# Performance work log

Hardware: AMD Instinct MI355X
Metric: run time of the kernel (lower is better)

Reference implementation:

```python
import jax, jax.numpy as jnp
import numpy as np

MAX_BITS = 64
HIDDEN = 256
EPS = 1e-5
TEMPERATURE = 1.0  # buffer default


def _layernorm(x, gamma, beta):
    mu = jnp.mean(x, axis=-1, keepdims=True)
    var = jnp.var(x, axis=-1, keepdims=True)
    return (x - mu) * jax.lax.rsqrt(var + EPS) * gamma + beta


def setup_inputs() -> dict:
    key = jax.random.key(0)
    ks = jax.random.split(key, 8)
    B = 32768
    # binary-ish inputs in [0,1)
    a_bits = (jax.random.uniform(ks[0], (B, MAX_BITS)) < 0.5).astype(jnp.float32)
    shift_bits = (jax.random.uniform(ks[1], (B, MAX_BITS)) < 0.5).astype(jnp.float32)
    # decoder: Linear(64,256) -> LN -> ReLU -> Linear(256,256) -> LN -> ReLU -> Linear(256,64)
    def lin(k, out_d, in_d):
        bound = 1.0 / np.sqrt(in_d)
        kw, kb = jax.random.split(k)
        W = jax.random.uniform(kw, (out_d, in_d), minval=-bound, maxval=bound)
        b = jax.random.uniform(kb, (out_d,), minval=-bound, maxval=bound)
        return W, b
    W1, b1 = lin(ks[2], HIDDEN, MAX_BITS)
    W2, b2 = lin(ks[3], HIDDEN, HIDDEN)
    W3, b3 = lin(ks[4], MAX_BITS, HIDDEN)
    g1 = jnp.ones((HIDDEN,)); be1 = jnp.zeros((HIDDEN,))
    g2 = jnp.ones((HIDDEN,)); be2 = jnp.zeros((HIDDEN,))
    return {
        "a_bits": a_bits, "shift_bits": shift_bits,
        "W1": W1, "b1": b1, "g1": g1, "be1": be1,
        "W2": W2, "b2": b2, "g2": g2, "be2": be2,
        "W3": W3, "b3": b3,
    }


def reference(a_bits, shift_bits, W1, b1, g1, be1, W2, b2, g2, be2, W3, b3):
    bits = a_bits.shape[1]
    # 2-layer MLP decoder
    h = jax.nn.relu(_layernorm(shift_bits @ W1.T + b1, g1, be1))
    h = jax.nn.relu(_layernorm(h @ W2.T + b2, g2, be2))
    shift_logits = (h @ W3.T + b3)[:, :bits]
    # training path: softmax over shift positions
    shift_probs = jax.nn.softmax(shift_logits / TEMPERATURE, axis=-1)
    # Toeplitz shift-sum: out[b,i] = sum_{s<=i} probs[b,s] * a_bits[b,i-s]
    i = jnp.arange(bits)[:, None]
    s = jnp.arange(bits)[None, :]
    idx = i - s                       # [bits, bits]
    mask = (idx >= 0)
    gath = a_bits[:, jnp.where(mask, idx, 0)] * mask.astype(a_bits.dtype)  # [B, bits, bits]
    return jnp.einsum('bis,bs->bi', gath, shift_probs)
```

## Files before the change

### kernel.cpp

```cpp
#include <hip/hip_runtime.h>
#include <hip/hip_fp16.h>


typedef short s8v __attribute__((ext_vector_type(8)));
typedef float f4v __attribute__((ext_vector_type(4)));

#define HPAD 264
#define PPAD 68

#define OFF_W1F 0
#define OFF_W2F 16384
#define OFF_W3F 81920
#define OFF_B1  98304
#define OFF_G1  98560
#define OFF_BE1 98816
#define OFF_B2  99072
#define OFF_G2  99328
#define OFF_BE2 99584
#define OFF_B3  99840

__device__ __forceinline__ float b2f(unsigned short u) {
    union { unsigned int i; float f; } v; v.i = ((unsigned int)u) << 16; return v.f;
}
__device__ __forceinline__ unsigned short f2b(float f) {
    union { float f; unsigned int i; } v; v.f = f;
    return (unsigned short)((v.i + 0x7fffu + ((v.i >> 16) & 1u)) >> 16);
}
__device__ __forceinline__ unsigned int cvtpk(float a, float b) {
    unsigned int r;
    asm("v_cvt_pk_bf16_f32 %0, %1, %2" : "=v"(r) : "v"(a), "v"(b));
    return r;
}
__device__ __forceinline__ int h2i(__half2 h) { union { __half2 h; int i; } u; u.h = h; return u.i; }
__device__ __forceinline__ __half2 i2h(int i) { union { __half2 h; int i; } u; u.i = i; return u.h; }

__device__ __forceinline__ bool probe_bf16(const void* a_bits) {
    unsigned int wv = ((const unsigned int*)a_bits)[threadIdx.x & 63];
    return __ballot((wv & 0xffffu) == 0x3f80u) != 0ULL;
}

__global__ __launch_bounds__(256) void convert_kernel(
    const void* __restrict__ a_probe,
    const void* __restrict__ W1, const void* __restrict__ W2, const void* __restrict__ W3,
    const void* __restrict__ b1, const void* __restrict__ g1, const void* __restrict__ be1,
    const void* __restrict__ b2, const void* __restrict__ g2, const void* __restrict__ be2,
    const void* __restrict__ b3,
    unsigned short* __restrict__ ws)
{
    const bool isbf = probe_bf16(a_probe);
    const int t = blockIdx.x * 256 + threadIdx.x;

    if (t < 12288) {
        const void* W; int K, idx, dstbase;
        if (t < 2048)       { idx = t;         W = W1; K = 64;  dstbase = OFF_W1F + idx * 8; }
        else if (t < 10240) { idx = t - 2048;  W = W2; K = 256; dstbase = OFF_W2F + idx * 8; }
        else                { idx = t - 10240; W = W3; K = 256; dstbase = OFF_W3F + idx * 8; }
        int nt, kc, lane;
        if (t < 2048) { nt = idx >> 7; kc = (idx >> 6) & 1; lane = idx & 63; }
        else          { nt = idx >> 9; kc = (idx >> 6) & 7; lane = idx & 63; }
        const int row = nt * 16 + (lane & 15);
        const int col = kc * 32 + (lane >> 4) * 8;
        const int src = row * K + col;
        s8v o;
        if (isbf) {
            o = *(const s8v*)((const unsigned short*)W + src);
        } else {
            const float* f = (const float*)W + src;
#pragma unroll
            for (int j = 0; j < 8; ++j) o[j] = (short)f2b(f[j]);
        }
        *(s8v*)(ws + dstbase) = o;
    } else if (t < 12488) {
        const int v = t - 12288;
        const void* srcp; int base, off;
        if (v < 32)       { srcp = b1;  base = OFF_B1;  off = v * 8; }
        else if (v < 64)  { srcp = g1;  base = OFF_G1;  off = (v - 32) * 8; }
        else if (v < 96)  { srcp = be1; base = OFF_BE1; off = (v - 64) * 8; }
        else if (v < 128) { srcp = b2;  base = OFF_B2;  off = (v - 96) * 8; }
        else if (v < 160) { srcp = g2;  base = OFF_G2;  off = (v - 128) * 8; }
        else if (v < 192) { srcp = be2; base = OFF_BE2; off = (v - 160) * 8; }
        else              { srcp = b3;  base = OFF_B3;  off = (v - 192) * 8; }
#pragma unroll
        for (int j = 0; j < 8; ++j)
            ws[base + off + j] = isbf ? ((const unsigned short*)srcp)[off + j]
                                      : f2b(((const float*)srcp)[off + j]);
    }
}

template<bool BF16>
__device__ __forceinline__ float loadS(const void* p, int idx) {
    if constexpr (BF16) return b2f(((const unsigned short*)p)[idx]);
    else return ((const float*)p)[idx];
}
template<bool BF16>
__device__ __forceinline__ s8v loadA8(const void* p, int idx) {
    if constexpr (BF16) {
        return *(const s8v*)((const unsigned short*)p + idx);
    } else {
        const float* f = (const float*)p + idx;
        f4v a = *(const f4v*)f;
        f4v b = *(const f4v*)(f + 4);
        union { s8v s; unsigned int u[4]; } r;
        r.u[0] = cvtpk(a[0], a[1]);
        r.u[1] = cvtpk(a[2], a[3]);
        r.u[2] = cvtpk(b[0], b[1]);
        r.u[3] = cvtpk(b[2], b[3]);
        return r.s;
    }
}
template<bool BF16>
__device__ __forceinline__ void storeO(void* p, int idx, float v) {
    if constexpr (BF16) ((unsigned short*)p)[idx] = f2b(v);
    else ((float*)p)[idx] = v;
}

__device__ __forceinline__ void ln_relu_store(
    f4v* acc, const unsigned short* ws, int offB, int offG, int offBe,
    short* Hs, float* SS, int w, int q, int c, int row, int ntb)
{
    float sm[4][4], sv[4][4];
#pragma unroll
    for (int mt = 0; mt < 4; ++mt)
#pragma unroll
        for (int r = 0; r < 4; ++r) { sm[mt][r] = 0.f; sv[mt][r] = 0.f; }
#pragma unroll
    for (int i = 0; i < 4; ++i) {
        const float bias = b2f(ws[offB + (ntb + i) * 16 + c]);
#pragma unroll
        for (int mt = 0; mt < 4; ++mt)
#pragma unroll
            for (int r = 0; r < 4; ++r) {
                float v = acc[mt * 4 + i][r] + bias;
                acc[mt * 4 + i][r] = v;
                sm[mt][r] += v; sv[mt][r] += v * v;
            }
    }
#pragma unroll
    for (int m = 1; m <= 8; m <<= 1)
#pragma unroll
        for (int mt = 0; mt < 4; ++mt)
#pragma unroll
            for (int r = 0; r < 4; ++r) {
                sm[mt][r] += __shfl_xor(sm[mt][r], m, 64);
                sv[mt][r] += __shfl_xor(sv[mt][r], m, 64);
            }
    if (c == 0)
#pragma unroll
        for (int mt = 0; mt < 4; ++mt)
#pragma unroll
            for (int r = 0; r < 4; ++r) {
                const int g = mt * 16 + row + r;
                *(float2*)&SS[g * 8 + w * 2] = make_float2(sm[mt][r], sv[mt][r]);
            }
    __syncthreads();
#pragma unroll
    for (int mt = 0; mt < 4; ++mt)
#pragma unroll
        for (int r = 0; r < 4; ++r) {
            const int g = mt * 16 + row + r;
            f4v v0 = *(const f4v*)&SS[g * 8];
            f4v v1 = *(const f4v*)&SS[g * 8 + 4];
            float st = v0[0] + v0[2] + v1[0] + v1[2];
            float sq = v0[1] + v0[3] + v1[1] + v1[3];
            float mean = st * (1.0f / 256.0f);
            float var  = fmaxf(sq * (1.0f / 256.0f) - mean * mean, 0.0f);
            sm[mt][r] = mean; sv[mt][r] = rsqrtf(var + 1e-5f);
        }
#pragma unroll
    for (int i = 0; i < 4; ++i) {
        const int nt = ntb + i;
        const float gg = b2f(ws[offG + nt * 16 + c]);
        const float bb = b2f(ws[offBe + nt * 16 + c]);
#pragma unroll
        for (int mt = 0; mt < 4; ++mt) {
            float y[4];
#pragma unroll
            for (int r = 0; r < 4; ++r)
                y[r] = fmaxf((acc[mt * 4 + i][r] - sm[mt][r]) * sv[mt][r] * gg + bb, 0.0f);
            unsigned int u01 = cvtpk(y[0], y[1]);
            unsigned int u23 = cvtpk(y[2], y[3]);
            Hs[(mt * 16 + row + 0) * HPAD + nt * 16 + c] = (short)(u01 & 0xffffu);
            Hs[(mt * 16 + row + 1) * HPAD + nt * 16 + c] = (short)(u01 >> 16);
            Hs[(mt * 16 + row + 2) * HPAD + nt * 16 + c] = (short)(u23 & 0xffffu);
            Hs[(mt * 16 + row + 3) * HPAD + nt * 16 + c] = (short)(u23 >> 16);
        }
    }
}

template<bool BF16>
__device__ __forceinline__ void pipeline(
    const void* a_bits, const void* shifts, const unsigned short* ws, void* out,
    short* Hs, float* Ps, float* SS)
{
    const int tid = threadIdx.x;
    const int w = tid >> 6;
    const int l = tid & 63;
    const int q = l >> 4;
    const int c = l & 15;
    const int ntb = w << 2;
    const int grow0 = (int)blockIdx.x << 6;
    const int row = q * 4;

    f4v acc1[16];
#pragma unroll
    for (int i = 0; i < 16; ++i) acc1[i] = (f4v){0.f, 0.f, 0.f, 0.f};

    s8v xa[4][2];
#pragma unroll
    for (int mt = 0; mt < 4; ++mt) {
        xa[mt][0] = loadA8<BF16>(shifts, (grow0 + mt * 16 + c) * 64 + q * 8);
        xa[mt][1] = loadA8<BF16>(shifts, (grow0 + mt * 16 + c) * 64 + 32 + q * 8);
    }
#pragma unroll
    for (int i = 0; i < 4; ++i) {
        const int nt = ntb + i;
        s8v wb0 = *(const s8v*)(ws + OFF_W1F + ((nt * 2 + 0) * 64 + l) * 8);
        s8v wb1 = *(const s8v*)(ws + OFF_W1F + ((nt * 2 + 1) * 64 + l) * 8);
#pragma unroll
        for (int mt = 0; mt < 4; ++mt) {
            acc1[mt * 4 + i] = __builtin_amdgcn_mfma_f32_16x16x32_bf16(xa[mt][0], wb0, acc1[mt * 4 + i], 0, 0, 0);
            acc1[mt * 4 + i] = __builtin_amdgcn_mfma_f32_16x16x32_bf16(xa[mt][1], wb1, acc1[mt * 4 + i], 0, 0, 0);
        }
    }
    ln_relu_store(acc1, ws, OFF_B1, OFF_G1, OFF_BE1, Hs, SS, w, q, c, row, ntb);
    __syncthreads();

    f4v acc2[16];
#pragma unroll
    for (int i = 0; i < 16; ++i) acc2[i] = (f4v){0.f, 0.f, 0.f, 0.f};
#pragma unroll
    for (int ks = 0; ks < 8; ++ks) {
        s8v af[4];
#pragma unroll
        for (int mt = 0; mt < 4; ++mt)
            af[mt] = *(const s8v*)&Hs[(mt * 16 + c) * HPAD + ks * 32 + q * 8];
#pragma unroll
        for (int i = 0; i < 4; ++i) {
            s8v bf_ = *(const s8v*)(ws + OFF_W2F + (((ntb + i) * 8 + ks) * 64 + l) * 8);
#pragma unroll
            for (int mt = 0; mt < 4; ++mt)
                acc2[mt * 4 + i] = __builtin_amdgcn_mfma_f32_16x16x32_bf16(af[mt], bf_, acc2[mt * 4 + i], 0, 0, 0);
        }
    }
    ln_relu_store(acc2, ws, OFF_B2, OFF_G2, OFF_BE2, Hs, SS, w, q, c, row, ntb);
    __syncthreads();

    f4v acc3[4];
#pragma unroll
    for (int t = 0; t < 4; ++t) acc3[t] = (f4v){0.f, 0.f, 0.f, 0.f};
#pragma unroll
    for (int ks = 0; ks < 8; ++ks) {
        s8v bf_ = *(const s8v*)(ws + OFF_W3F + ((w * 8 + ks) * 64 + l) * 8);
#pragma unroll
        for (int mt = 0; mt < 4; ++mt) {
            s8v af = *(const s8v*)&Hs[(mt * 16 + c) * HPAD + ks * 32 + q * 8];
            acc3[mt] = __builtin_amdgcn_mfma_f32_16x16x32_bf16(af, bf_, acc3[mt], 0, 0, 0);
        }
    }
    {
        const float bias = b2f(ws[OFF_B3 + w * 16 + c]);
        float sum[4][4];
#pragma unroll
        for (int mt = 0; mt < 4; ++mt)
#pragma unroll
            for (int r = 0; r < 4; ++r) {
                float e = __expf(acc3[mt][r] + bias);
                Ps[(mt * 16 + row + r) * PPAD + w * 16 + c] = e;
                sum[mt][r] = e;
            }
#pragma unroll
        for (int m = 1; m <= 8; m <<= 1)
#pragma unroll
            for (int mt = 0; mt < 4; ++mt)
#pragma unroll
                for (int r = 0; r < 4; ++r)
                    sum[mt][r] += __shfl_xor(sum[mt][r], m, 64);
        if (c == 0)
#pragma unroll
            for (int mt = 0; mt < 4; ++mt)
#pragma unroll
                for (int r = 0; r < 4; ++r)
                    SS[(mt * 16 + row + r) * 8 + w * 2 + 1] = sum[mt][r];
    }
    __syncthreads();

#pragma unroll
    for (int jj = 0; jj < 8; ++jj) {
        const int m0 = w * 16 + jj;
        const int m1 = m0 + 8;
        f4v u0 = *(const f4v*)&SS[m0 * 8];
        f4v u1 = *(const f4v*)&SS[m0 * 8 + 4];
        f4v u2 = *(const f4v*)&SS[m1 * 8];
        f4v u3 = *(const f4v*)&SS[m1 * 8 + 4];
        const float i0 = __builtin_amdgcn_rcpf(u0[1] + u0[3] + u1[1] + u1[3]);
        const float i1 = __builtin_amdgcn_rcpf(u2[1] + u2[3] + u3[1] + u3[3]);
        __half2 pph = __floats2half2_rn(Ps[m0 * PPAD + l] * i0,
                                        Ps[m1 * PPAD + l] * i1);
        const int ppi = h2i(pph);
        __half2 aah = __floats2half2_rn(loadS<BF16>(a_bits, (grow0 + m0) * 64 + l),
                                        loadS<BF16>(a_bits, (grow0 + m1) * 64 + l));
        int rr = h2i(aah);
        __half2 acc = __float2half2_rn(0.0f);
#pragma unroll
        for (int s = 0; s < 64; ++s) {
            const int spi = __builtin_amdgcn_readlane(ppi, s);
            acc = __hfma2(i2h(spi), i2h(rr), acc);
            if (s < 63)
                rr = __builtin_amdgcn_update_dpp(0, rr, 0x138, 0xF, 0xF, true);
        }
        storeO<BF16>(out, (grow0 + m0) * 64 + l, __low2float(acc));
        storeO<BF16>(out, (grow0 + m1) * 64 + l, __high2float(acc));
    }
}

__global__ __launch_bounds__(256, 3) void shiftdec_kernel(
    const void* __restrict__ a_bits, const void* __restrict__ shifts,
    const unsigned short* __restrict__ ws, void* __restrict__ out)
{
    __shared__ __align__(16) short Hs[64 * HPAD];
    __shared__ __align__(16) float Ps[64 * PPAD];
    __shared__ __align__(16) float SSb[64 * 8];

    if (probe_bf16(a_bits))
        pipeline<true>(a_bits, shifts, ws, out, Hs, Ps, SSb);
    else
        pipeline<false>(a_bits, shifts, ws, out, Hs, Ps, SSb);
}

extern "C" void kernel_launch(void* const* d_in, const int* in_sizes, int n_in,
                              void* d_out, int out_size, void* d_ws, size_t ws_size,
                              hipStream_t stream) {
    const int B = in_sizes[0] / 64;
    const int grid = B / 64;

    hipLaunchKernelGGL(convert_kernel, dim3(49), dim3(256), 0, stream,
                       d_in[0], d_in[2], d_in[6], d_in[10],
                       d_in[3], d_in[4], d_in[5], d_in[7], d_in[8], d_in[9], d_in[11],
                       (unsigned short*)d_ws);
    hipLaunchKernelGGL(shiftdec_kernel, dim3(grid), dim3(256), 0, stream,
                       d_in[0], d_in[1], (const unsigned short*)d_ws, d_out);
}
```

Baseline: 123.2 us.

## Split each 64-row tile across eight waves instead of four

Doubles the block to 512 threads so each wave owns two output column tiles instead of four in the two hidden layers. The last layer is split by column tile and row pair, and the shift-sum loop covers fewer rows per wave. LayerNorm partial stats now combine eight waves, and the softmax sums use a new shared buffer. This halves accumulator registers per thread to raise occupancy and parallelism per tile. The cost is more cross-wave reduction and barrier traffic, and each wave reuses the loaded A fragments over fewer MFMAs.

After: 132.0 us. 1.07x slower.

```diff
diff --git a/kernel.cpp b/kernel.cpp
--- a/kernel.cpp
+++ b/kernel.cpp
@@ -124,14 +124,14 @@
 #pragma unroll
         for (int r = 0; r < 4; ++r) { sm[mt][r] = 0.f; sv[mt][r] = 0.f; }
 #pragma unroll
-    for (int i = 0; i < 4; ++i) {
+    for (int i = 0; i < 2; ++i) {
         const float bias = b2f(ws[offB + (ntb + i) * 16 + c]);
 #pragma unroll
         for (int mt = 0; mt < 4; ++mt)
 #pragma unroll
             for (int r = 0; r < 4; ++r) {
-                float v = acc[mt * 4 + i][r] + bias;
-                acc[mt * 4 + i][r] = v;
+                float v = acc[mt * 2 + i][r] + bias;
+                acc[mt * 2 + i][r] = v;
                 sm[mt][r] += v; sv[mt][r] += v * v;
             }
     }
@@ -150,7 +150,7 @@
 #pragma unroll
             for (int r = 0; r < 4; ++r) {
                 const int g = mt * 16 + row + r;
-                *(float2*)&SS[g * 8 + w * 2] = make_float2(sm[mt][r], sv[mt][r]);
+                *(float2*)&SS[g * 16 + w * 2] = make_float2(sm[mt][r], sv[mt][r]);
             }
     __syncthreads();
 #pragma unroll
@@ -158,16 +158,18 @@
 #pragma unroll
         for (int r = 0; r < 4; ++r) {
             const int g = mt * 16 + row + r;
-            f4v v0 = *(const f4v*)&SS[g * 8];
-            f4v v1 = *(const f4v*)&SS[g * 8 + 4];
-            float st = v0[0] + v0[2] + v1[0] + v1[2];
-            float sq = v0[1] + v0[3] + v1[1] + v1[3];
+            f4v v0 = *(const f4v*)&SS[g * 16];
+            f4v v1 = *(const f4v*)&SS[g * 16 + 4];
+            f4v v2 = *(const f4v*)&SS[g * 16 + 8];
+            f4v v3 = *(const f4v*)&SS[g * 16 + 12];
+            float st = (v0[0] + v0[2]) + (v1[0] + v1[2]) + (v2[0] + v2[2]) + (v3[0] + v3[2]);
+            float sq = (v0[1] + v0[3]) + (v1[1] + v1[3]) + (v2[1] + v2[3]) + (v3[1] + v3[3]);
             float mean = st * (1.0f / 256.0f);
             float var  = fmaxf(sq * (1.0f / 256.0f) - mean * mean, 0.0f);
             sm[mt][r] = mean; sv[mt][r] = rsqrtf(var + 1e-5f);
         }
 #pragma unroll
-    for (int i = 0; i < 4; ++i) {
+    for (int i = 0; i < 2; ++i) {
         const int nt = ntb + i;
         const float gg = b2f(ws[offG + nt * 16 + c]);
         const float bb = b2f(ws[offBe + nt * 16 + c]);
@@ -176,7 +178,7 @@
             float y[4];
 #pragma unroll
             for (int r = 0; r < 4; ++r)
-                y[r] = fmaxf((acc[mt * 4 + i][r] - sm[mt][r]) * sv[mt][r] * gg + bb, 0.0f);
+                y[r] = fmaxf((acc[mt * 2 + i][r] - sm[mt][r]) * sv[mt][r] * gg + bb, 0.0f);
             unsigned int u01 = cvtpk(y[0], y[1]);
             unsigned int u23 = cvtpk(y[2], y[3]);
             Hs[(mt * 16 + row + 0) * HPAD + nt * 16 + c] = (short)(u01 & 0xffffu);
@@ -190,20 +192,20 @@
 template<bool BF16>
 __device__ __forceinline__ void pipeline(
     const void* a_bits, const void* shifts, const unsigned short* ws, void* out,
-    short* Hs, float* Ps, float* SS)
+    short* Hs, float* Ps, float* SS, float* SM)
 {
     const int tid = threadIdx.x;
     const int w = tid >> 6;
     const int l = tid & 63;
     const int q = l >> 4;
     const int c = l & 15;
-    const int ntb = w << 2;
+    const int ntb = w << 1;
     const int grow0 = (int)blockIdx.x << 6;
     const int row = q * 4;
 
-    f4v acc1[16];
-#pragma unroll
-    for (int i = 0; i < 16; ++i) acc1[i] = (f4v){0.f, 0.f, 0.f, 0.f};
+    f4v acc1[8];
+#pragma unroll
+    for (int i = 0; i < 8; ++i) acc1[i] = (f4v){0.f, 0.f, 0.f, 0.f};
 
     s8v xa[4][2];
 #pragma unroll
@@ -212,22 +214,22 @@
         xa[mt][1] = loadA8<BF16>(shifts, (grow0 + mt * 16 + c) * 64 + 32 + q * 8);
     }
 #pragma unroll
-    for (int i = 0; i < 4; ++i) {
+    for (int i = 0; i < 2; ++i) {
         const int nt = ntb + i;
         s8v wb0 = *(const s8v*)(ws + OFF_W1F + ((nt * 2 + 0) * 64 + l) * 8);
         s8v wb1 = *(const s8v*)(ws + OFF_W1F + ((nt * 2 + 1) * 64 + l) * 8);
 #pragma unroll
         for (int mt = 0; mt < 4; ++mt) {
-            acc1[mt * 4 + i] = __builtin_amdgcn_mfma_f32_16x16x32_bf16(xa[mt][0], wb0, acc1[mt * 4 + i], 0, 0, 0);
-            acc1[mt * 4 + i] = __builtin_amdgcn_mfma_f32_16x16x32_bf16(xa[mt][1], wb1, acc1[mt * 4 + i], 0, 0, 0);
+            acc1[mt * 2 + i] = __builtin_amdgcn_mfma_f32_16x16x32_bf16(xa[mt][0], wb0, acc1[mt * 2 + i], 0, 0, 0);
+            acc1[mt * 2 + i] = __builtin_amdgcn_mfma_f32_16x16x32_bf16(xa[mt][1], wb1, acc1[mt * 2 + i], 0, 0, 0);
         }
     }
     ln_relu_store(acc1, ws, OFF_B1, OFF_G1, OFF_BE1, Hs, SS, w, q, c, row, ntb);
     __syncthreads();
 
-    f4v acc2[16];
-#pragma unroll
-    for (int i = 0; i < 16; ++i) acc2[i] = (f4v){0.f, 0.f, 0.f, 0.f};
+    f4v acc2[8];
+#pragma unroll
+    for (int i = 0; i < 8; ++i) acc2[i] = (f4v){0.f, 0.f, 0.f, 0.f};
 #pragma unroll
     for (int ks = 0; ks < 8; ++ks) {
         s8v af[4];
@@ -235,65 +237,68 @@
         for (int mt = 0; mt < 4; ++mt)
             af[mt] = *(const s8v*)&Hs[(mt * 16 + c) * HPAD + ks * 32 + q * 8];
 #pragma unroll
-        for (int i = 0; i < 4; ++i) {
+        for (int i = 0; i < 2; ++i) {
             s8v bf_ = *(const s8v*)(ws + OFF_W2F + (((ntb + i) * 8 + ks) * 64 + l) * 8);
 #pragma unroll
             for (int mt = 0; mt < 4; ++mt)
-                acc2[mt * 4 + i] = __builtin_amdgcn_mfma_f32_16x16x32_bf16(af[mt], bf_, acc2[mt * 4 + i], 0, 0, 0);
+                acc2[mt * 2 + i] = __builtin_amdgcn_mfma_f32_16x16x32_bf16(af[mt], bf_, acc2[mt * 2 + i], 0, 0, 0);
         }
     }
     ln_relu_store(acc2, ws, OFF_B2, OFF_G2, OFF_BE2, Hs, SS, w, q, c, row, ntb);
     __syncthreads();
 
-    f4v acc3[4];
-#pragma unroll
-    for (int t = 0; t < 4; ++t) acc3[t] = (f4v){0.f, 0.f, 0.f, 0.f};
+    const int nt3 = w & 3;
+    const int p = w >> 2;
+    f4v acc3[2];
+#pragma unroll
+    for (int t = 0; t < 2; ++t) acc3[t] = (f4v){0.f, 0.f, 0.f, 0.f};
 #pragma unroll
     for (int ks = 0; ks < 8; ++ks) {
-        s8v bf_ = *(const s8v*)(ws + OFF_W3F + ((w * 8 + ks) * 64 + l) * 8);
-#pragma unroll
-        for (int mt = 0; mt < 4; ++mt) {
-            s8v af = *(const s8v*)&Hs[(mt * 16 + c) * HPAD + ks * 32 + q * 8];
-            acc3[mt] = __builtin_amdgcn_mfma_f32_16x16x32_bf16(af, bf_, acc3[mt], 0, 0, 0);
+        s8v bf_ = *(const s8v*)(ws + OFF_W3F + ((nt3 * 8 + ks) * 64 + l) * 8);
+#pragma unroll
+        for (int t = 0; t < 2; ++t) {
+            s8v af = *(const s8v*)&Hs[((p * 2 + t) * 16 + c) * HPAD + ks * 32 + q * 8];
+            acc3[t] = __builtin_amdgcn_mfma_f32_16x16x32_bf16(af, bf_, acc3[t], 0, 0, 0);
         }
     }
     {
-        const float bias = b2f(ws[OFF_B3 + w * 16 + c]);
-        float sum[4][4];
-#pragma unroll
-        for (int mt = 0; mt < 4; ++mt)
+        const float bias = b2f(ws[OFF_B3 + nt3 * 16 + c]);
+        float sum[2][4];
+#pragma unroll
+        for (int t = 0; t < 2; ++t)
 #pragma unroll
             for (int r = 0; r < 4; ++r) {
-                float e = __expf(acc3[mt][r] + bias);
-                Ps[(mt * 16 + row + r) * PPAD + w * 16 + c] = e;
-                sum[mt][r] = e;
+                float e = __expf(acc3[t][r] + bias);
+                const int g = (p * 2 + t) * 16 + row + r;
+                Ps[g * PPAD + nt3 * 16 + c] = e;
+                sum[t][r] = e;
             }
 #pragma unroll
         for (int m = 1; m <= 8; m <<= 1)
 #pragma unroll
-            for (int mt = 0; mt < 4; ++mt)
+            for (int t = 0; t < 2; ++t)
 #pragma unroll
                 for (int r = 0; r < 4; ++r)
-                    sum[mt][r] += __shfl_xor(sum[mt][r], m, 64);
+                    sum[t][r] += __shfl_xor(sum[t][r], m, 64);
         if (c == 0)
 #pragma unroll
-            for (int mt = 0; mt < 4; ++mt)
-#pragma unroll
-                for (int r = 0; r < 4; ++r)
-                    SS[(mt * 16 + row + r) * 8 + w * 2 + 1] = sum[mt][r];
+            for (int t = 0; t < 2; ++t)
+#pragma unroll
+                for (int r = 0; r < 4; ++r) {
+                    const int g = (p * 2 + t) * 16 + row + r;
+                    SM[g * 4 + nt3] = sum[t][r];
+                }
     }
     __syncthreads();
 
 #pragma unroll
-    for (int jj = 0; jj < 8; ++jj) {
-        const int m0 = w * 16 + jj;
-        const int m1 = m0 + 8;
-        f4v u0 = *(const f4v*)&SS[m0 * 8];
-        f4v u1 = *(const f4v*)&SS[m0 * 8 + 4];
-        f4v u2 = *(const f4v*)&SS[m1 * 8];
-        f4v u3 = *(const f4v*)&SS[m1 * 8 + 4];
-        const float i0 = __builtin_amdgcn_rcpf(u0[1] + u0[3] + u1[1] + u1[3]);
-        const float i1 = __builtin_amdgcn_rcpf(u2[1] + u2[3] + u3[1] + u3[3]);
+    for (int jj = 0; jj < 4; ++jj) {
+        const int m0 = w * 8 + jj;
+        const int m1 = m0 + 4;
+        f4v u0 = *(const f4v*)&SM[m0 * 4];
+        f4v u1 = *(const f4v*)&SM[m1 * 4];
+        const float i0 = __builtin_amdgcn_rcpf(u0[0] + u0[1] + u0[2] + u0[3]);
+        const float i1 = __builtin_amdgcn_rcpf(u1[0] + u1[1] + u1[2] + u1[3]);
         __half2 pph = __floats2half2_rn(Ps[m0 * PPAD + l] * i0,
                                         Ps[m1 * PPAD + l] * i1);
         const int ppi = h2i(pph);
@@ -313,18 +318,19 @@
     }
 }
 
-__global__ __launch_bounds__(256, 3) void shiftdec_kernel(
+__global__ __launch_bounds__(512, 4) void shiftdec_kernel(
     const void* __restrict__ a_bits, const void* __restrict__ shifts,
     const unsigned short* __restrict__ ws, void* __restrict__ out)
 {
     __shared__ __align__(16) short Hs[64 * HPAD];
     __shared__ __align__(16) float Ps[64 * PPAD];
-    __shared__ __align__(16) float SSb[64 * 8];
+    __shared__ __align__(16) float SSb[64 * 16];
+    __shared__ __align__(16) float SMb[64 * 4];
 
     if (probe_bf16(a_bits))
-        pipeline<true>(a_bits, shifts, ws, out, Hs, Ps, SSb);
+        pipeline<true>(a_bits, shifts, ws, out, Hs, Ps, SSb, SMb);
     else
-        pipeline<false>(a_bits, shifts, ws, out, Hs, Ps, SSb);
+        pipeline<false>(a_bits, shifts, ws, out, Hs, Ps, SSb, SMb);
 }
 
 extern "C" void kernel_launch(void* const* d_in, const int* in_sizes, int n_in,
@@ -337,6 +343,6 @@
                        d_in[0], d_in[2], d_in[6], d_in[10],
                        d_in[3], d_in[4], d_in[5], d_in[7], d_in[8], d_in[9], d_in[11],
                        (unsigned short*)d_ws);
-    hipLaunchKernelGGL(shiftdec_kernel, dim3(grid), dim3(256), 0, stream,
+    hipLaunchKernelGGL(shiftdec_kernel, dim3(grid), dim3(512), 0, stream,
                        d_in[0], d_in[1], (const unsigned short*)d_ws, d_out);
 }
```
